# Kernel tuning notes

Measured on AMD Instinct MI355X. Metric: run time of the kernel, lower is better.

Reference implementation:

```python
import jax, jax.numpy as jnp
import numpy as np

D = 1024
H = 16
HD = D // H  # 64
BASE = 10000.0


def _rope_tables(seq_len, dtype=jnp.float32):
    # inv_freq over even dims, rotate-half convention: emb = cat(freqs, freqs)
    inv_freq = 1.0 / (BASE ** (jnp.arange(0, HD, 2, dtype=jnp.float32) / HD))
    t = jnp.arange(seq_len, dtype=jnp.float32)
    freqs = jnp.einsum('i,j->ij', t, inv_freq)          # [S, HD/2]
    emb = jnp.concatenate([freqs, freqs], axis=-1)       # [S, HD]
    return jnp.cos(emb).astype(dtype), jnp.sin(emb).astype(dtype)


def _rotate_half(x):
    x1, x2 = jnp.split(x, 2, axis=-1)
    return jnp.concatenate([-x2, x1], axis=-1)


def setup_inputs() -> dict:
    key = jax.random.key(0)
    ks = jax.random.split(key, 5)
    B, S = 2, 2048
    scale = 0.02
    return {
        'x': jax.random.normal(ks[0], (B, S, D), dtype=jnp.float32),
        'wq': jax.random.normal(ks[1], (D, D), dtype=jnp.float32) * scale,
        'wk': jax.random.normal(ks[2], (D, D), dtype=jnp.float32) * scale,
        'wv': jax.random.normal(ks[3], (D, D), dtype=jnp.float32) * scale,
        'wo': jax.random.normal(ks[4], (D, D), dtype=jnp.float32) * scale,
    }


def reference(x, wq, wk, wv, wo):
    B, S, _ = x.shape
    # QKV projections (torch Linear: x @ W^T), split into heads -> [B, H, S, HD]
    def proj(w):
        return jnp.einsum('bsd,ed->bse', x, w).reshape(B, S, H, HD).transpose(0, 2, 1, 3)
    q, k, v = proj(wq), proj(wk), proj(wv)

    # RoPE (rotate-half)
    cos, sin = _rope_tables(S, x.dtype)                  # [S, HD]
    cos = cos[None, None, :, :]
    sin = sin[None, None, :, :]
    q = q * cos + _rotate_half(q) * sin
    k = k * cos + _rotate_half(k) * sin

    # causal scaled-dot-product attention
    scores = jnp.einsum('bhqd,bhkd->bhqk', q, k) / jnp.sqrt(jnp.array(HD, x.dtype))
    causal = jnp.tril(jnp.ones((S, S), dtype=bool))
    scores = jnp.where(causal[None, None], scores, jnp.finfo(x.dtype).min)
    attn = jax.nn.softmax(scores, axis=-1)
    out = jnp.einsum('bhqk,bhkd->bhqd', attn, v)         # [B, H, S, HD]

    out = out.transpose(0, 2, 1, 3).reshape(B, S, D)
    return jnp.einsum('bsd,ed->bse', out, wo)
```

## Files before the change

### kernel.cpp

```cpp
#include <hip/hip_runtime.h>
#include <cstdint>
#include <cstddef>

typedef unsigned short u16;
typedef unsigned int u32;
typedef __bf16 bf16x8 __attribute__((ext_vector_type(8)));
typedef float f32x4 __attribute__((ext_vector_type(4)));
typedef u16 u16x8 __attribute__((ext_vector_type(8)));
typedef u16 u16x4 __attribute__((ext_vector_type(4)));

#define DD 1024
#define HH 16
#define HDIM 64
#define BB 2
#define SS 2048
#define MM (BB * SS)
#define NQT 32

__device__ __forceinline__ u16 cvt(float f) {
  __bf16 h = (__bf16)f;
  return __builtin_bit_cast(u16, h);
}
__device__ __forceinline__ f32x4 mfma16(bf16x8 a, bf16x8 b, f32x4 c) {
  return __builtin_amdgcn_mfma_f32_16x16x32_bf16(a, b, c, 0, 0, 0);
}
__device__ __forceinline__ bf16x8 ld_bf8(const u16* p) {
  return __builtin_bit_cast(bf16x8, *(const u16x8*)p);
}
__device__ __forceinline__ void async16(const void* g, void* l) {
  __builtin_amdgcn_global_load_lds(
      (__attribute__((address_space(1))) void*)(uintptr_t)g,
      (__attribute__((address_space(3))) void*)l, 16, 0, 0);
}

__global__ void cast_all(const float* __restrict__ x, const float* __restrict__ wq,
                         const float* __restrict__ wk, const float* __restrict__ wv,
                         const float* __restrict__ wo, u16* __restrict__ xb,
                         u16* __restrict__ wqb, u16* __restrict__ wkb,
                         u16* __restrict__ wvb, u16* __restrict__ wob) {
  int i = blockIdx.x * 256 + threadIdx.x;
  const float* src;
  u16* dst;
  int off;
  if (i < (1 << 20)) {
    src = x; dst = xb; off = i;
  } else {
    int j = i - (1 << 20);
    int w = j >> 18;
    off = j & ((1 << 18) - 1);
    src = (w == 0) ? wq : (w == 1) ? wk : (w == 2) ? wv : wo;
    dst = (w == 0) ? wqb : (w == 1) ? wkb : (w == 2) ? wvb : wob;
  }
  float4 v = ((const float4*)src)[off];
  u16x4 o;
  o[0] = cvt(v.x); o[1] = cvt(v.y); o[2] = cvt(v.z); o[3] = cvt(v.w);
  *(u16x4*)&dst[(size_t)off * 4] = o;
}

__global__ __launch_bounds__(256) void gemm_qkv(
    const u16* __restrict__ xb, const u16* __restrict__ wq,
    const u16* __restrict__ wk, const u16* __restrict__ wv,
    u16* __restrict__ Qo, u16* __restrict__ Ko, u16* __restrict__ Vto) {
  __shared__ __align__(16) u16 As[128 * 32];
  __shared__ __align__(16) u16 Bs[128 * 32];
  const int t = threadIdx.x;
  const int w = t >> 6, l = t & 63, lane16 = l & 15, quad = l >> 4;
  const int m0 = blockIdx.x * 128, n0 = blockIdx.y * 128;
  const u16* wsel = (blockIdx.z == 0) ? wq : (blockIdx.z == 1) ? wk : wv;
  const int m_w = (w >> 1) * 64, n_w = (w & 1) * 64;
  const int srow = t >> 2, scol = (t & 3) * 8;

  f32x4 acc[4][4] = {};
  for (int kt = 0; kt < 32; ++kt) {
    const int k0 = kt * 32;
    async16(&xb[(size_t)(m0 + srow) * DD + k0 + scol], &As[t * 8]);
    async16(&xb[(size_t)(m0 + 64 + srow) * DD + k0 + scol], &As[2048 + t * 8]);
    async16(&wsel[(size_t)(n0 + srow) * DD + k0 + scol], &Bs[t * 8]);
    async16(&wsel[(size_t)(n0 + 64 + srow) * DD + k0 + scol], &Bs[2048 + t * 8]);
    __syncthreads();
    bf16x8 af[4], bfr[4];
#pragma unroll
    for (int mi = 0; mi < 4; ++mi)
      af[mi] = ld_bf8(&As[(m_w + mi * 16 + lane16) * 32 + quad * 8]);
#pragma unroll
    for (int ni = 0; ni < 4; ++ni)
      bfr[ni] = ld_bf8(&Bs[(n_w + ni * 16 + lane16) * 32 + quad * 8]);
#pragma unroll
    for (int mi = 0; mi < 4; ++mi)
#pragma unroll
      for (int ni = 0; ni < 4; ++ni)
        acc[mi][ni] = mfma16(af[mi], bfr[ni], acc[mi][ni]);
    __syncthreads();
  }
  if (blockIdx.z == 2) {
#pragma unroll
    for (int mi = 0; mi < 4; ++mi) {
      int mbase = m0 + m_w + mi * 16 + quad * 4;
      int b = mbase >> 11, s0 = mbase & (SS - 1);
#pragma unroll
      for (int ni = 0; ni < 4; ++ni) {
        int e = n0 + n_w + ni * 16 + lane16;
        int h = e >> 6, d = e & 63;
        u16x4 pk;
#pragma unroll
        for (int r = 0; r < 4; ++r) pk[r] = cvt(acc[mi][ni][r]);
        *(u16x4*)&Vto[((size_t)(b * HH + h) * HDIM + d) * SS + s0] = pk;
      }
    }
  } else {
    u16* osel = (blockIdx.z == 0) ? Qo : Ko;
    const float scale = (blockIdx.z == 0) ? 0.18033688f : 1.0f;
    float invf[2];
    invf[0] = exp2f((float)lane16 * -0.4152410119f) * 0.15915494309f;
    invf[1] = exp2f((float)(16 + lane16) * -0.4152410119f) * 0.15915494309f;
    const int h = (n0 + n_w) >> 6;
#pragma unroll
    for (int mi = 0; mi < 4; ++mi) {
#pragma unroll
      for (int r = 0; r < 4; ++r) {
        int mrow = m0 + m_w + mi * 16 + quad * 4 + r;
        int b = mrow >> 11, s = mrow & (SS - 1);
        size_t rowbase = ((size_t)(b * HH + h) * SS + s) * HDIM;
#pragma unroll
        for (int ni = 0; ni < 2; ++ni) {
          float x1 = acc[mi][ni][r], x2 = acc[mi][ni + 2][r];
          float rv = (float)s * invf[ni];
          rv = rv - floorf(rv);
          float sn = __builtin_amdgcn_sinf(rv);
          float c  = __builtin_amdgcn_cosf(rv);
          int d = ni * 16 + lane16;
          osel[rowbase + d]      = cvt((x1 * c - x2 * sn) * scale);
          osel[rowbase + d + 32] = cvt((x2 * c + x1 * sn) * scale);
        }
      }
    }
  }
}

__global__ __launch_bounds__(256, 2) void attn_k(const u16* __restrict__ Qb,
                                                 const u16* __restrict__ Kb,
                                                 const u16* __restrict__ Vt,
                                                 u16* __restrict__ AO) {
  __shared__ __align__(16) u16 KsF[2][128 * 64];
  __shared__ __align__(16) u16 VtL[2][64 * 128];
  __shared__ __align__(16) u16 Ps[4][16 * 128];
  const int t = threadIdx.x;
  const int w = t >> 6, l = t & 63, lane16 = l & 15, quad = l >> 4;
  const int bh = blockIdx.x;
  const int jj = NQT - 1 - (int)blockIdx.y;
  const size_t base = (size_t)bh * SS * HDIM;
  const u16* Qp = Qb + base;
  const int b = bh >> 4, h = bh & 15;

  const int q0 = jj * 64;
  const int qrow = q0 + w * 16 + lane16;
  bf16x8 qf0 = ld_bf8(&Qp[(size_t)qrow * 64 + quad * 8]);
  bf16x8 qf1 = ld_bf8(&Qp[(size_t)qrow * 64 + 32 + quad * 8]);

  u16x8 onesu;
#pragma unroll
  for (int i = 0; i < 8; ++i) onesu[i] = 0x3F80;
  const bf16x8 ones = __builtin_bit_cast(bf16x8, onesu);

  f32x4 o[4] = {};
  f32x4 lacc = {};

  const u16* kptr[4];
  const u16* vptr[4];
#pragma unroll
  for (int i = 0; i < 4; ++i) {
    int p = i * 256 + t;
    int r = p >> 3;
    int c = (p & 7) ^ (r & 7);
    kptr[i] = Kb + base + (size_t)r * 64 + c * 8;
    int d = p >> 4;
    int q = (p & 15) ^ (d & 15);
    vptr[i] = Vt + base + (size_t)d * SS + q * 8;
  }

#pragma unroll
  for (int i = 0; i < 4; ++i) {
    async16(kptr[i], &KsF[0][(i * 256 + t) * 8]);
    kptr[i] += 128 * 64;
    async16(vptr[i], &VtL[0][(i * 256 + t) * 8]);
    vptr[i] += 128;
  }

  u16* Pw = Ps[w];
  const int ktmax = jj >> 1;
  for (int kt = 0; kt <= ktmax; ++kt) {
    __syncthreads();
    if (kt < ktmax) {
      const int nb = (kt + 1) & 1;
#pragma unroll
      for (int i = 0; i < 4; ++i) {
        async16(kptr[i], &KsF[nb][(i * 256 + t) * 8]);
        kptr[i] += 128 * 64;
        async16(vptr[i], &VtL[nb][(i * 256 + t) * 8]);
        vptr[i] += 128;
      }
    }
    const u16* Kc = KsF[kt & 1];
    const u16* Vc = VtL[kt & 1];
    const int kv0 = kt * 128;
    f32x4 st[8];
#pragma unroll
    for (int nc = 0; nc < 8; ++nc) {
      int rr = nc * 16 + lane16;
      int p0 = rr * 8 + (quad ^ (rr & 7));
      int p1 = rr * 8 + ((4 + quad) ^ (rr & 7));
      f32x4 a = {0.f, 0.f, 0.f, 0.f};
      a = mfma16(ld_bf8(&Kc[p0 * 8]), qf0, a);
      a = mfma16(ld_bf8(&Kc[p1 * 8]), qf1, a);
      st[nc] = a;
    }
    if (kt == ktmax) {
#pragma unroll
      for (int nc = 0; nc < 8; ++nc) {
        int kvb = kv0 + nc * 16 + quad * 4;
#pragma unroll
        for (int r = 0; r < 4; ++r)
          if (kvb + r > qrow) st[nc][r] = -3.0e38f;
      }
    }
#pragma unroll
    for (int nc = 0; nc < 8; ++nc)
#pragma unroll
      for (int r = 0; r < 4; ++r) st[nc][r] = exp2f(st[nc][r]);
#pragma unroll
    for (int nc = 0; nc < 8; ++nc) {
      u16x4 pk;
#pragma unroll
      for (int r = 0; r < 4; ++r) pk[r] = cvt(st[nc][r]);
      int addr = lane16 * 128 + (((nc * 2 + (quad >> 1)) ^ lane16) * 8) + (quad & 1) * 4;
      *(u16x4*)&Pw[addr] = pk;
    }
#pragma unroll
    for (int G = 0; G < 4; ++G) {
      int gc = ((G * 4 + quad) ^ lane16) * 8;
      bf16x8 pf = ld_bf8(&Pw[lane16 * 128 + gc]);
      lacc = mfma16(ones, pf, lacc);
#pragma unroll
      for (int nd = 0; nd < 4; ++nd) {
        int d = nd * 16 + lane16;
        bf16x8 bv = ld_bf8(&Vc[(size_t)d * 128 + gc]);
        o[nd] = mfma16(bv, pf, o[nd]);
      }
    }
  }
  const float inv = 1.0f / lacc[0];
  const size_t rowb = (size_t)(b * SS + qrow) * DD + h * HDIM + quad * 4;
#pragma unroll
  for (int nd = 0; nd < 4; ++nd) {
    u16x4 pk;
#pragma unroll
    for (int r = 0; r < 4; ++r) pk[r] = cvt(o[nd][r] * inv);
    *(u16x4*)&AO[rowb + nd * 16] = pk;
  }
}

__global__ __launch_bounds__(256) void gemm_out(const u16* __restrict__ A, const u16* __restrict__ W,
                                                float* __restrict__ out) {
  __shared__ __align__(16) u16 As[128 * 32];
  __shared__ __align__(16) u16 Bs[64 * 32];
  const int t = threadIdx.x;
  const int w = t >> 6, l = t & 63, lane16 = l & 15, quad = l >> 4;
  const int m0 = blockIdx.x * 128, n0 = blockIdx.y * 64;
  const int m_w = (w >> 1) * 64, n_w = (w & 1) * 32;
  const int srow = t >> 2, scol = (t & 3) * 8;

  f32x4 acc[4][2] = {};
  for (int kt = 0; kt < 32; ++kt) {
    const int k0 = kt * 32;
    async16(&A[(size_t)(m0 + srow) * DD + k0 + scol], &As[t * 8]);
    async16(&A[(size_t)(m0 + 64 + srow) * DD + k0 + scol], &As[2048 + t * 8]);
    async16(&W[(size_t)(n0 + srow) * DD + k0 + scol], &Bs[t * 8]);
    __syncthreads();
    bf16x8 af[4], bfr[2];
#pragma unroll
    for (int mi = 0; mi < 4; ++mi)
      af[mi] = ld_bf8(&As[(m_w + mi * 16 + lane16) * 32 + quad * 8]);
#pragma unroll
    for (int ni = 0; ni < 2; ++ni)
      bfr[ni] = ld_bf8(&Bs[(n_w + ni * 16 + lane16) * 32 + quad * 8]);
#pragma unroll
    for (int mi = 0; mi < 4; ++mi)
#pragma unroll
      for (int ni = 0; ni < 2; ++ni)
        acc[mi][ni] = mfma16(af[mi], bfr[ni], acc[mi][ni]);
    __syncthreads();
  }
#pragma unroll
  for (int mi = 0; mi < 4; ++mi) {
#pragma unroll
    for (int r = 0; r < 4; ++r) {
      int mrow = m0 + m_w + mi * 16 + quad * 4 + r;
#pragma unroll
      for (int ni = 0; ni < 2; ++ni) {
        int e = n0 + n_w + ni * 16 + lane16;
        out[(size_t)mrow * DD + e] = acc[mi][ni][r];
      }
    }
  }
}

extern "C" void kernel_launch(void* const* d_in, const int* in_sizes, int n_in,
                              void* d_out, int out_size, void* d_ws, size_t ws_size,
                              hipStream_t stream) {
  const float* x  = (const float*)d_in[0];
  const float* wq = (const float*)d_in[1];
  const float* wk = (const float*)d_in[2];
  const float* wv = (const float*)d_in[3];
  const float* wo = (const float*)d_in[4];
  float* out = (float*)d_out;
  char* ws = (char*)d_ws;

  u16* xb  = (u16*)(ws + (size_t)0);
  u16* wqb = (u16*)(ws + ((size_t)8  << 20));
  u16* wkb = (u16*)(ws + ((size_t)10 << 20));
  u16* wvb = (u16*)(ws + ((size_t)12 << 20));
  u16* wob = (u16*)(ws + ((size_t)14 << 20));
  u16* Qb  = (u16*)(ws + ((size_t)16 << 20));
  u16* Kb  = (u16*)(ws + ((size_t)24 << 20));
  u16* Vtg = (u16*)(ws + ((size_t)32 << 20));
  u16* AO  = (u16*)(ws + ((size_t)40 << 20));

  cast_all<<<8192, 256, 0, stream>>>(x, wq, wk, wv, wo, xb, wqb, wkb, wvb, wob);
  gemm_qkv<<<dim3(32, 8, 3), 256, 0, stream>>>(xb, wqb, wkb, wvb, Qb, Kb, Vtg);
  attn_k<<<dim3(32, 32), 256, 0, stream>>>(Qb, Kb, Vtg, AO);
  gemm_out<<<dim3(32, 16), 256, 0, stream>>>(AO, wob, out);
}
```

Measured before the change: 168.5 us.

## Double query rows per attention block, single-buffer K/V, split P into halves

Each attention block now handles 128 query rows (32 per wave, two 16-row groups), so each K/V tile loaded into LDS is reused for twice as many queries and the grid is halved. K/V double buffering is dropped in favor of single LDS buffers with load-then-sync. The P tile is processed in two 64-column halves to shrink LDS, and the occupancy hint is raised to 3 blocks per CU. The cost is that global loads no longer overlap compute, per-thread register use goes up, and the causal tail is coarser.

```diff
diff --git a/kernel.cpp b/kernel.cpp
--- a/kernel.cpp
+++ b/kernel.cpp
@@ -15,7 +15,6 @@
 #define BB 2
 #define SS 2048
 #define MM (BB * SS)
-#define NQT 32
 
 __device__ __forceinline__ u16 cvt(float f) {
   __bf16 h = (__bf16)f;
@@ -137,33 +136,38 @@
   }
 }
 
-__global__ __launch_bounds__(256, 2) void attn_k(const u16* __restrict__ Qb,
+__global__ __launch_bounds__(256, 3) void attn_k(const u16* __restrict__ Qb,
                                                  const u16* __restrict__ Kb,
                                                  const u16* __restrict__ Vt,
                                                  u16* __restrict__ AO) {
-  __shared__ __align__(16) u16 KsF[2][128 * 64];
-  __shared__ __align__(16) u16 VtL[2][64 * 128];
-  __shared__ __align__(16) u16 Ps[4][16 * 128];
+  __shared__ __align__(16) u16 KsF[128 * 64];
+  __shared__ __align__(16) u16 VtL[64 * 128];
+  __shared__ __align__(16) u16 Ps[4][32 * 64];
   const int t = threadIdx.x;
   const int w = t >> 6, l = t & 63, lane16 = l & 15, quad = l >> 4;
   const int bh = blockIdx.x;
-  const int jj = NQT - 1 - (int)blockIdx.y;
+  const int jj = 15 - (int)blockIdx.y;
   const size_t base = (size_t)bh * SS * HDIM;
   const u16* Qp = Qb + base;
   const int b = bh >> 4, h = bh & 15;
 
-  const int q0 = jj * 64;
-  const int qrow = q0 + w * 16 + lane16;
-  bf16x8 qf0 = ld_bf8(&Qp[(size_t)qrow * 64 + quad * 8]);
-  bf16x8 qf1 = ld_bf8(&Qp[(size_t)qrow * 64 + 32 + quad * 8]);
+  const int q0 = jj * 128;
+  int qrw[2];
+  bf16x8 qf[2][2];
+#pragma unroll
+  for (int g = 0; g < 2; ++g) {
+    qrw[g] = q0 + w * 32 + g * 16 + lane16;
+    qf[g][0] = ld_bf8(&Qp[(size_t)qrw[g] * 64 + quad * 8]);
+    qf[g][1] = ld_bf8(&Qp[(size_t)qrw[g] * 64 + 32 + quad * 8]);
+  }
 
   u16x8 onesu;
 #pragma unroll
   for (int i = 0; i < 8; ++i) onesu[i] = 0x3F80;
   const bf16x8 ones = __builtin_bit_cast(bf16x8, onesu);
 
-  f32x4 o[4] = {};
-  f32x4 lacc = {};
+  f32x4 o[2][4] = {};
+  f32x4 lacc[2] = {};
 
   const u16* kptr[4];
   const u16* vptr[4];
@@ -178,84 +182,74 @@
     vptr[i] = Vt + base + (size_t)d * SS + q * 8;
   }
 
-#pragma unroll
-  for (int i = 0; i < 4; ++i) {
-    async16(kptr[i], &KsF[0][(i * 256 + t) * 8]);
-    kptr[i] += 128 * 64;
-    async16(vptr[i], &VtL[0][(i * 256 + t) * 8]);
-    vptr[i] += 128;
-  }
-
   u16* Pw = Ps[w];
-  const int ktmax = jj >> 1;
+  const int ktmax = jj;
   for (int kt = 0; kt <= ktmax; ++kt) {
-    __syncthreads();
-    if (kt < ktmax) {
-      const int nb = (kt + 1) & 1;
-#pragma unroll
-      for (int i = 0; i < 4; ++i) {
-        async16(kptr[i], &KsF[nb][(i * 256 + t) * 8]);
-        kptr[i] += 128 * 64;
-        async16(vptr[i], &VtL[nb][(i * 256 + t) * 8]);
-        vptr[i] += 128;
-      }
-    }
-    const u16* Kc = KsF[kt & 1];
-    const u16* Vc = VtL[kt & 1];
+#pragma unroll
+    for (int i = 0; i < 4; ++i) {
+      async16(kptr[i], &KsF[(i * 256 + t) * 8]);
+      kptr[i] += 128 * 64;
+      async16(vptr[i], &VtL[(i * 256 + t) * 8]);
+      vptr[i] += 128;
+    }
+    __syncthreads();
     const int kv0 = kt * 128;
-    f32x4 st[8];
-#pragma unroll
-    for (int nc = 0; nc < 8; ++nc) {
-      int rr = nc * 16 + lane16;
-      int p0 = rr * 8 + (quad ^ (rr & 7));
-      int p1 = rr * 8 + ((4 + quad) ^ (rr & 7));
-      f32x4 a = {0.f, 0.f, 0.f, 0.f};
-      a = mfma16(ld_bf8(&Kc[p0 * 8]), qf0, a);
-      a = mfma16(ld_bf8(&Kc[p1 * 8]), qf1, a);
-      st[nc] = a;
-    }
-    if (kt == ktmax) {
-#pragma unroll
-      for (int nc = 0; nc < 8; ++nc) {
-        int kvb = kv0 + nc * 16 + quad * 4;
-#pragma unroll
-        for (int r = 0; r < 4; ++r)
-          if (kvb + r > qrow) st[nc][r] = -3.0e38f;
-      }
-    }
-#pragma unroll
-    for (int nc = 0; nc < 8; ++nc)
-#pragma unroll
-      for (int r = 0; r < 4; ++r) st[nc][r] = exp2f(st[nc][r]);
-#pragma unroll
-    for (int nc = 0; nc < 8; ++nc) {
+#pragma unroll
+    for (int kh = 0; kh < 2; ++kh) {
+#pragma unroll
+      for (int nci = 0; nci < 4; ++nci) {
+        const int nc = kh * 4 + nci;
+        const int rr = nc * 16 + lane16;
+        bf16x8 k0 = ld_bf8(&KsF[(rr * 8 + (quad ^ (rr & 7))) * 8]);
+        bf16x8 k1 = ld_bf8(&KsF[(rr * 8 + ((4 + quad) ^ (rr & 7))) * 8]);
+        const int kvb = kv0 + nc * 16 + quad * 4;
+#pragma unroll
+        for (int g = 0; g < 2; ++g) {
+          f32x4 a = {0.f, 0.f, 0.f, 0.f};
+          a = mfma16(k0, qf[g][0], a);
+          a = mfma16(k1, qf[g][1], a);
+          if (kt == ktmax) {
+#pragma unroll
+            for (int r = 0; r < 4; ++r)
+              if (kvb + r > qrw[g]) a[r] = -3.0e38f;
+          }
+          u16x4 pk;
+#pragma unroll
+          for (int r = 0; r < 4; ++r) pk[r] = cvt(exp2f(a[r]));
+          int addr = (g * 16 + lane16) * 64 +
+                     (((nci * 2 + (quad >> 1)) ^ (lane16 & 7)) * 8) + (quad & 1) * 4;
+          *(u16x4*)&Pw[addr] = pk;
+        }
+      }
+#pragma unroll
+      for (int cf = 0; cf < 2; ++cf) {
+        const int cidx = ((cf * 4 + quad) ^ (lane16 & 7)) * 8;
+        bf16x8 pfA = ld_bf8(&Pw[lane16 * 64 + cidx]);
+        bf16x8 pfB = ld_bf8(&Pw[(16 + lane16) * 64 + cidx]);
+        lacc[0] = mfma16(ones, pfA, lacc[0]);
+        lacc[1] = mfma16(ones, pfB, lacc[1]);
+        const int gch = ((kh * 8 + cf * 4 + quad) ^ lane16) * 8;
+#pragma unroll
+        for (int nd = 0; nd < 4; ++nd) {
+          bf16x8 bv = ld_bf8(&VtL[(size_t)(nd * 16 + lane16) * 128 + gch]);
+          o[0][nd] = mfma16(bv, pfA, o[0][nd]);
+          o[1][nd] = mfma16(bv, pfB, o[1][nd]);
+        }
+      }
+    }
+    __syncthreads();
+  }
+#pragma unroll
+  for (int g = 0; g < 2; ++g) {
+    const float inv = 1.0f / lacc[g][0];
+    const size_t rowb = (size_t)(b * SS + qrw[g]) * DD + h * HDIM + quad * 4;
+#pragma unroll
+    for (int nd = 0; nd < 4; ++nd) {
       u16x4 pk;
 #pragma unroll
-      for (int r = 0; r < 4; ++r) pk[r] = cvt(st[nc][r]);
-      int addr = lane16 * 128 + (((nc * 2 + (quad >> 1)) ^ lane16) * 8) + (quad & 1) * 4;
-      *(u16x4*)&Pw[addr] = pk;
-    }
-#pragma unroll
-    for (int G = 0; G < 4; ++G) {
-      int gc = ((G * 4 + quad) ^ lane16) * 8;
-      bf16x8 pf = ld_bf8(&Pw[lane16 * 128 + gc]);
-      lacc = mfma16(ones, pf, lacc);
-#pragma unroll
-      for (int nd = 0; nd < 4; ++nd) {
-        int d = nd * 16 + lane16;
-        bf16x8 bv = ld_bf8(&Vc[(size_t)d * 128 + gc]);
-        o[nd] = mfma16(bv, pf, o[nd]);
-      }
-    }
-  }
-  const float inv = 1.0f / lacc[0];
-  const size_t rowb = (size_t)(b * SS + qrow) * DD + h * HDIM + quad * 4;
-#pragma unroll
-  for (int nd = 0; nd < 4; ++nd) {
-    u16x4 pk;
-#pragma unroll
-    for (int r = 0; r < 4; ++r) pk[r] = cvt(o[nd][r] * inv);
-    *(u16x4*)&AO[rowb + nd * 16] = pk;
+      for (int r = 0; r < 4; ++r) pk[r] = cvt(o[g][nd][r] * inv);
+      *(u16x4*)&AO[rowb + nd * 16] = pk;
+    }
   }
 }
 
@@ -327,6 +321,6 @@
 
   cast_all<<<8192, 256, 0, stream>>>(x, wq, wk, wv, wo, xb, wqb, wkb, wvb, wob);
   gemm_qkv<<<dim3(32, 8, 3), 256, 0, stream>>>(xb, wqb, wkb, wvb, Qb, Kb, Vtg);
-  attn_k<<<dim3(32, 32), 256, 0, stream>>>(Qb, Kb, Vtg, AO);
+  attn_k<<<dim3(32, 16), 256, 0, stream>>>(Qb, Kb, Vtg, AO);
   gemm_out<<<dim3(32, 16), 256, 0, stream>>>(AO, wob, out);
 }
```

Result: slower. 179.1 us (+6.3%).
